# Kernel optimization log

Measured on AMD Instinct MI355X. Metric: run time of the kernel, lower is better.

Reference implementation:

```python
import jax, jax.numpy as jnp
import numpy as np

EPS = 1e-5

def _act_quant(x):
    # per-token int8 absmax quantization with straight-through estimator
    scale = 127.0 / jnp.clip(jnp.max(jnp.abs(x), axis=-1, keepdims=True), EPS, None)
    q = jnp.clip(jnp.round(x * scale), -128.0, 127.0) / scale
    return x + jax.lax.stop_gradient(q - x)

def _weight_quant(w):
    # per-tensor ternary (1.58-bit) quantization with STE
    scale = 1.0 / jnp.clip(jnp.mean(jnp.abs(w)), EPS, None)
    q = jnp.clip(jnp.round(w * scale), -1.0, 1.0) / scale
    return w + jax.lax.stop_gradient(q - w)

def _bitlinear(x, w, b):
    y = jnp.einsum('bsd,od->bso', _act_quant(x), _weight_quant(w))
    return y + b

def setup_inputs() -> dict:
    key = jax.random.key(0)
    k1, k2, k3, k4, k5 = jax.random.split(key, 5)
    B, S, D, F = 8, 4096, 1024, 3072
    return {
        'x': jax.random.normal(k1, (B, S, D), dtype=jnp.float32),
        'up_w': jax.random.normal(k2, (F, D), dtype=jnp.float32) * 0.125,
        'up_b': jax.random.normal(k3, (F,), dtype=jnp.float32) * 0.01,
        'down_w': jax.random.normal(k4, (D, F), dtype=jnp.float32) * 0.125,
        'down_b': jax.random.normal(k5, (D,), dtype=jnp.float32) * 0.01,
    }

def reference(x, up_w, up_b, down_w, down_b):
    hidden = _bitlinear(x, up_w, up_b)          # [B,S,3072]
    hidden = jnp.square(jax.nn.relu(hidden))    # relu(h)^2
    return _bitlinear(hidden, down_w, down_b)   # [B,S,1024]
```

## Files before the change

kernel.cpp:

```cpp
#include <hip/hip_runtime.h>
#include <hip/hip_bf16.h>
#include <stdint.h>

#define EPS 1e-5f

typedef int v4i __attribute__((ext_vector_type(4)));
typedef int v16i __attribute__((ext_vector_type(16)));
typedef const __attribute__((address_space(1))) void g_void;
typedef __attribute__((address_space(3))) void l_void;

__device__ inline float block_max_nw(float v, int nw) {
    __shared__ float s[8];
#pragma unroll
    for (int o = 32; o; o >>= 1) v = fmaxf(v, __shfl_xor(v, o, 64));
    if ((threadIdx.x & 63) == 0) s[threadIdx.x >> 6] = v;
    __syncthreads();
    float m = s[0];
    for (int i = 1; i < nw; ++i) m = fmaxf(m, s[i]);
    return m;
}

__device__ inline float block_sum64x4(float v) {
    __shared__ float s[4];
#pragma unroll
    for (int o = 32; o; o >>= 1) v += __shfl_xor(v, o, 64);
    if ((threadIdx.x & 63) == 0) s[threadIdx.x >> 6] = v;
    __syncthreads();
    return s[0] + s[1] + s[2] + s[3];
}

__global__ __launch_bounds__(256) void abs_sum_part_k(const float4* __restrict__ w,
                                                      int n4, float* __restrict__ part) {
    float s = 0.0f;
    for (int i = blockIdx.x * 256 + threadIdx.x; i < n4; i += 1024 * 256) {
        float4 v = w[i];
        s += fabsf(v.x) + fabsf(v.y) + fabsf(v.z) + fabsf(v.w);
    }
    s = block_sum64x4(s);
    if (threadIdx.x == 0) part[blockIdx.x] = s;
}

__global__ __launch_bounds__(256) void abs_sum_final_k(const float* __restrict__ parts,
                                                       float* __restrict__ sums) {
    const float* p = parts + blockIdx.x * 1024;
    const int t = threadIdx.x;
    float s = p[t] + p[t + 256] + p[t + 512] + p[t + 768];
    s = block_sum64x4(s);
    if (t == 0) sums[blockIdx.x] = s;
}

__global__ __launch_bounds__(256) void wquant_k(const float4* __restrict__ w,
                                                char4* __restrict__ q,
                                                const float* __restrict__ sum) {
    const float mean = fmaxf(sum[0] * (1.0f / 3145728.0f), EPS);
    const float scale = 1.0f / mean;
    const int i = blockIdx.x * 256 + threadIdx.x;
    float4 v = w[i];
    char4 c;
    c.x = (signed char)(int)fmaxf(fminf(rintf(v.x * scale), 1.0f), -1.0f);
    c.y = (signed char)(int)fmaxf(fminf(rintf(v.y * scale), 1.0f), -1.0f);
    c.z = (signed char)(int)fmaxf(fminf(rintf(v.z * scale), 1.0f), -1.0f);
    c.w = (signed char)(int)fmaxf(fminf(rintf(v.w * scale), 1.0f), -1.0f);
    q[i] = c;
}

__global__ __launch_bounds__(256) void aquant_k(const float4* __restrict__ x,
                                                char4* __restrict__ q,
                                                float* __restrict__ deq) {
    const int row = blockIdx.x, t = threadIdx.x;
    const float4 v = x[(size_t)row * 256 + t];
    float m = fmaxf(fmaxf(fabsf(v.x), fabsf(v.y)), fmaxf(fabsf(v.z), fabsf(v.w)));
    m = block_max_nw(m, 4);
    const float mc = fmaxf(m, EPS);
    const float sc = 127.0f / mc;
    char4 c;
    c.x = (signed char)(int)fmaxf(fminf(rintf(v.x * sc), 127.0f), -128.0f);
    c.y = (signed char)(int)fmaxf(fminf(rintf(v.y * sc), 127.0f), -128.0f);
    c.z = (signed char)(int)fmaxf(fminf(rintf(v.z * sc), 127.0f), -128.0f);
    c.w = (signed char)(int)fmaxf(fminf(rintf(v.w * sc), 127.0f), -128.0f);
    q[(size_t)row * 256 + t] = c;
    if (t == 0) deq[row] = mc / 127.0f;
}

__global__ __launch_bounds__(384) void hquant_k(unsigned short* __restrict__ hid,
                                                float* __restrict__ deq) {
    const size_t row = blockIdx.x;
    const int t = threadIdx.x;
    unsigned short* rp = hid + row * 3072;
    const uint4 u = ((const uint4*)rp)[t];
    float v[8];
    {
        uint32_t uu[4] = {u.x, u.y, u.z, u.w};
#pragma unroll
        for (int i = 0; i < 4; ++i) {
            uint32_t lo = uu[i] << 16, hi = uu[i] & 0xFFFF0000u;
            v[2 * i]     = __uint_as_float(lo);
            v[2 * i + 1] = __uint_as_float(hi);
        }
    }
    float m = 0.0f;
#pragma unroll
    for (int i = 0; i < 8; ++i) m = fmaxf(m, fabsf(v[i]));
    m = block_max_nw(m, 6);
    const float mc = fmaxf(m, EPS);
    const float sc = 127.0f / mc;
    uint32_t p0 = 0, p1 = 0;
#pragma unroll
    for (int i = 0; i < 4; ++i) {
        int c = (int)fminf(rintf(v[i] * sc), 127.0f);
        p0 |= (uint32_t)(c & 255) << (8 * i);
    }
#pragma unroll
    for (int i = 0; i < 4; ++i) {
        int c = (int)fminf(rintf(v[4 + i] * sc), 127.0f);
        p1 |= (uint32_t)(c & 255) << (8 * i);
    }
    uint2 pk; pk.x = p0; pk.y = p1;
    ((uint2*)rp)[t] = pk;
    if (t == 0) deq[row] = mc / 127.0f;
}

template <bool RELU2, typename OutT>
__global__ __launch_bounds__(256, 2) void gemm_i8(
    const int8_t* __restrict__ A, int lda,
    const int8_t* __restrict__ B, int ldb,
    OutT* __restrict__ O, int ldo,
    const float* __restrict__ rowDeq,
    const float* __restrict__ sumPtr,
    const float* __restrict__ bias,
    int K, int nTiles) {
    __shared__ __align__(16) char As[128 * 128];
    __shared__ __align__(16) char Bs[256 * 128];
    const int t = threadIdx.x;
    const int lane = t & 63;
    const int w = t >> 6;
    const int xcd = blockIdx.x & 7;
    const int s = blockIdx.x >> 3;
    const int bm = xcd + 8 * (s / nTiles);
    const int bn = s % nTiles;
    const long m0 = (long)bm * 128;
    const long n0 = (long)bn * 256;

    v16i acc[2][4];
#pragma unroll
    for (int i = 0; i < 2; ++i)
#pragma unroll
        for (int j = 0; j < 4; ++j) acc[i][j] = (v16i)(0);

    const int mloc = (w >> 1) * 64;
    const int nloc = (w & 1) * 128;
    const int r32 = lane & 31;
    const int h = lane >> 5;
    const int swz = r32 & 7;
    const int srow = lane >> 3;
    const int scol = ((lane & 7) ^ srow) * 16;

    const int8_t* pa = A + (m0 + w * 8 + srow) * (long)lda + scol;
    const int8_t* pb = B + (n0 + w * 8 + srow) * (long)ldb + scol;

    int cs[4];
#pragma unroll
    for (int ks = 0; ks < 4; ++ks) cs[ks] = ((ks * 2 + h) ^ swz) * 16;

    for (int k0 = 0; k0 < K; k0 += 128) {
#pragma unroll
        for (int r = 0; r < 4; ++r)
            __builtin_amdgcn_global_load_lds((g_void*)(pa + (long)r * 32 * lda + k0),
                                             (l_void*)(As + r * 4096 + w * 1024), 16, 0, 0);
#pragma unroll
        for (int r = 0; r < 8; ++r)
            __builtin_amdgcn_global_load_lds((g_void*)(pb + (long)r * 32 * ldb + k0),
                                             (l_void*)(Bs + r * 4096 + w * 1024), 16, 0, 0);
        __syncthreads();
#pragma unroll
        for (int ks = 0; ks < 4; ++ks) {
            v4i af[2], bf[4];
#pragma unroll
            for (int mt = 0; mt < 2; ++mt)
                af[mt] = *(const v4i*)(As + (mloc + mt * 32 + r32) * 128 + cs[ks]);
#pragma unroll
            for (int nt = 0; nt < 4; ++nt)
                bf[nt] = *(const v4i*)(Bs + (nloc + nt * 32 + r32) * 128 + cs[ks]);
#pragma unroll
            for (int mt = 0; mt < 2; ++mt)
#pragma unroll
                for (int nt = 0; nt < 4; ++nt)
                    acc[mt][nt] = __builtin_amdgcn_mfma_i32_32x32x32_i8(
                        af[mt], bf[nt], acc[mt][nt], 0, 0, 0);
        }
        __syncthreads();
    }

    const float wdeq = fmaxf(sumPtr[0] * (1.0f / 3145728.0f), EPS);
#pragma unroll
    for (int mt = 0; mt < 2; ++mt) {
#pragma unroll
        for (int g = 0; g < 4; ++g) {
#pragma unroll
            for (int rr = 0; rr < 4; ++rr) {
                const long row = m0 + mloc + mt * 32 + g * 8 + h * 4 + rr;
                const float rs = rowDeq[row] * wdeq;
#pragma unroll
                for (int nt = 0; nt < 4; ++nt) {
                    const long col = n0 + nloc + nt * 32 + r32;
                    float val = (float)acc[mt][nt][g * 4 + rr] * rs + bias[col];
                    if (RELU2) {
                        val = fmaxf(val, 0.0f);
                        val = val * val;
                    }
                    O[row * (long)ldo + col] = (OutT)val;
                }
            }
        }
    }
}

extern "C" void kernel_launch(void* const* d_in, const int* in_sizes, int n_in,
                              void* d_out, int out_size, void* d_ws, size_t ws_size,
                              hipStream_t stream) {
    const float* x      = (const float*)d_in[0];
    const float* up_w   = (const float*)d_in[1];
    const float* up_b   = (const float*)d_in[2];
    const float* down_w = (const float*)d_in[3];
    const float* down_b = (const float*)d_in[4];

    char* ws = (char*)d_ws;
    float*  sums   = (float*)ws;
    float*  parts  = (float*)(ws + 256);
    int8_t* qw_dn  = (int8_t*)(ws + 256 + 8192);
    float*  deqh   = (float*)(ws + 256 + 8192 + 3145728);
    __hip_bfloat16* hidden = (__hip_bfloat16*)(ws + 256 + 8192 + 3145728 + 131072);

    int8_t* qx    = (int8_t*)d_out;
    int8_t* qw_up = qx + 33554432;
    float*  deqx  = (float*)(qx + 33554432 + 3145728);

    abs_sum_part_k<<<1024, 256, 0, stream>>>((const float4*)up_w, 786432, parts);
    abs_sum_part_k<<<1024, 256, 0, stream>>>((const float4*)down_w, 786432, parts + 1024);
    abs_sum_final_k<<<2, 256, 0, stream>>>(parts, sums);

    wquant_k<<<3072, 256, 0, stream>>>((const float4*)up_w, (char4*)qw_up, &sums[0]);
    wquant_k<<<3072, 256, 0, stream>>>((const float4*)down_w, (char4*)qw_dn, &sums[1]);
    aquant_k<<<32768, 256, 0, stream>>>((const float4*)x, (char4*)qx, deqx);

    gemm_i8<true, __hip_bfloat16><<<3072, 256, 0, stream>>>(
        qx, 1024, qw_up, 1024, hidden, 3072, deqx, &sums[0], up_b, 1024, 12);
    hquant_k<<<32768, 384, 0, stream>>>((unsigned short*)hidden, deqh);
    gemm_i8<false, float><<<1024, 256, 0, stream>>>(
        (const int8_t*)hidden, 6144, qw_dn, 3072, (float*)d_out, 1024,
        deqh, &sums[1], down_b, 3072, 4);
}
```

Measured before the change: 537.6 us.

## Enlarge int8 GEMM tile to 256x256 with 8 waves and double-buffered LDS prefetch

```diff
diff --git a/kernel.cpp b/kernel.cpp
--- a/kernel.cpp
+++ b/kernel.cpp
@@ -121,7 +121,7 @@
 }
 
 template <bool RELU2, typename OutT>
-__global__ __launch_bounds__(256, 2) void gemm_i8(
+__global__ __launch_bounds__(512, 2) void gemm_i8(
     const int8_t* __restrict__ A, int lda,
     const int8_t* __restrict__ B, int ldb,
     OutT* __restrict__ O, int ldo,
@@ -129,31 +129,33 @@
     const float* __restrict__ sumPtr,
     const float* __restrict__ bias,
     int K, int nTiles) {
-    __shared__ __align__(16) char As[128 * 128];
-    __shared__ __align__(16) char Bs[256 * 128];
+    __shared__ __align__(16) char As[2][32768];
+    __shared__ __align__(16) char Bs[2][32768];
     const int t = threadIdx.x;
     const int lane = t & 63;
     const int w = t >> 6;
+    const int wm = w >> 2;
+    const int wn = w & 3;
     const int xcd = blockIdx.x & 7;
-    const int s = blockIdx.x >> 3;
-    const int bm = xcd + 8 * (s / nTiles);
-    const int bn = s % nTiles;
-    const long m0 = (long)bm * 128;
+    const int sb = blockIdx.x >> 3;
+    const int bm = xcd + 8 * (sb / nTiles);
+    const int bn = sb % nTiles;
+    const long m0 = (long)bm * 256;
     const long n0 = (long)bn * 256;
 
-    v16i acc[2][4];
-#pragma unroll
-    for (int i = 0; i < 2; ++i)
-#pragma unroll
-        for (int j = 0; j < 4; ++j) acc[i][j] = (v16i)(0);
-
-    const int mloc = (w >> 1) * 64;
-    const int nloc = (w & 1) * 128;
+    v16i acc[4][2];
+#pragma unroll
+    for (int i = 0; i < 4; ++i)
+#pragma unroll
+        for (int j = 0; j < 2; ++j) acc[i][j] = (v16i)(0);
+
     const int r32 = lane & 31;
     const int h = lane >> 5;
     const int swz = r32 & 7;
     const int srow = lane >> 3;
     const int scol = ((lane & 7) ^ srow) * 16;
+    const int mloc = wm * 128;
+    const int nloc = wn * 64;
 
     const int8_t* pa = A + (m0 + w * 8 + srow) * (long)lda + scol;
     const int8_t* pb = B + (n0 + w * 8 + srow) * (long)ldb + scol;
@@ -162,38 +164,62 @@
 #pragma unroll
     for (int ks = 0; ks < 4; ++ks) cs[ks] = ((ks * 2 + h) ^ swz) * 16;
 
-    for (int k0 = 0; k0 < K; k0 += 128) {
+    const int NT = K >> 7;
+
+    auto STAGE = [&](int tt, int buf) {
+        const long ko = (long)tt << 7;
 #pragma unroll
         for (int r = 0; r < 4; ++r)
-            __builtin_amdgcn_global_load_lds((g_void*)(pa + (long)r * 32 * lda + k0),
-                                             (l_void*)(As + r * 4096 + w * 1024), 16, 0, 0);
-#pragma unroll
-        for (int r = 0; r < 8; ++r)
-            __builtin_amdgcn_global_load_lds((g_void*)(pb + (long)r * 32 * ldb + k0),
-                                             (l_void*)(Bs + r * 4096 + w * 1024), 16, 0, 0);
-        __syncthreads();
+            __builtin_amdgcn_global_load_lds((g_void*)(pa + (long)(r * 64) * lda + ko),
+                                             (l_void*)(As[buf] + r * 8192 + w * 1024), 16, 0, 0);
+#pragma unroll
+        for (int r = 0; r < 4; ++r)
+            __builtin_amdgcn_global_load_lds((g_void*)(pb + (long)(r * 64) * ldb + ko),
+                                             (l_void*)(Bs[buf] + r * 8192 + w * 1024), 16, 0, 0);
+    };
+
+    STAGE(0, 0);
+    STAGE(1, 1);
+    asm volatile("s_waitcnt vmcnt(8)" ::: "memory");
+    __builtin_amdgcn_s_barrier();
+    asm volatile("" ::: "memory");
+
+    for (int tt = 0; tt < NT; ++tt) {
+        const int cur = tt & 1;
+        v4i af[4][4], bf[2][4];
 #pragma unroll
         for (int ks = 0; ks < 4; ++ks) {
-            v4i af[2], bf[4];
-#pragma unroll
-            for (int mt = 0; mt < 2; ++mt)
-                af[mt] = *(const v4i*)(As + (mloc + mt * 32 + r32) * 128 + cs[ks]);
-#pragma unroll
-            for (int nt = 0; nt < 4; ++nt)
-                bf[nt] = *(const v4i*)(Bs + (nloc + nt * 32 + r32) * 128 + cs[ks]);
-#pragma unroll
-            for (int mt = 0; mt < 2; ++mt)
-#pragma unroll
-                for (int nt = 0; nt < 4; ++nt)
+#pragma unroll
+            for (int mt = 0; mt < 4; ++mt)
+                af[mt][ks] = *(const v4i*)(As[cur] + (mloc + mt * 32 + r32) * 128 + cs[ks]);
+#pragma unroll
+            for (int nt = 0; nt < 2; ++nt)
+                bf[nt][ks] = *(const v4i*)(Bs[cur] + (nloc + nt * 32 + r32) * 128 + cs[ks]);
+        }
+        asm volatile("s_waitcnt lgkmcnt(0)" ::: "memory");
+        __builtin_amdgcn_s_barrier();
+        asm volatile("" ::: "memory");
+        const bool pf = (tt + 2 < NT);
+        if (pf) STAGE(tt + 2, cur);
+        __builtin_amdgcn_s_setprio(1);
+#pragma unroll
+        for (int ks = 0; ks < 4; ++ks)
+#pragma unroll
+            for (int mt = 0; mt < 4; ++mt)
+#pragma unroll
+                for (int nt = 0; nt < 2; ++nt)
                     acc[mt][nt] = __builtin_amdgcn_mfma_i32_32x32x32_i8(
-                        af[mt], bf[nt], acc[mt][nt], 0, 0, 0);
-        }
-        __syncthreads();
+                        af[mt][ks], bf[nt][ks], acc[mt][nt], 0, 0, 0);
+        __builtin_amdgcn_s_setprio(0);
+        if (pf) asm volatile("s_waitcnt vmcnt(8)" ::: "memory");
+        else    asm volatile("s_waitcnt vmcnt(0)" ::: "memory");
+        __builtin_amdgcn_s_barrier();
+        asm volatile("" ::: "memory");
     }
 
     const float wdeq = fmaxf(sumPtr[0] * (1.0f / 3145728.0f), EPS);
 #pragma unroll
-    for (int mt = 0; mt < 2; ++mt) {
+    for (int mt = 0; mt < 4; ++mt) {
 #pragma unroll
         for (int g = 0; g < 4; ++g) {
 #pragma unroll
@@ -201,7 +227,7 @@
                 const long row = m0 + mloc + mt * 32 + g * 8 + h * 4 + rr;
                 const float rs = rowDeq[row] * wdeq;
 #pragma unroll
-                for (int nt = 0; nt < 4; ++nt) {
+                for (int nt = 0; nt < 2; ++nt) {
                     const long col = n0 + nloc + nt * 32 + r32;
                     float val = (float)acc[mt][nt][g * 4 + rr] * rs + bias[col];
                     if (RELU2) {
@@ -243,10 +269,10 @@
     wquant_k<<<3072, 256, 0, stream>>>((const float4*)down_w, (char4*)qw_dn, &sums[1]);
     aquant_k<<<32768, 256, 0, stream>>>((const float4*)x, (char4*)qx, deqx);
 
-    gemm_i8<true, __hip_bfloat16><<<3072, 256, 0, stream>>>(
+    gemm_i8<true, __hip_bfloat16><<<1536, 512, 0, stream>>>(
         qx, 1024, qw_up, 1024, hidden, 3072, deqx, &sums[0], up_b, 1024, 12);
     hquant_k<<<32768, 384, 0, stream>>>((unsigned short*)hidden, deqh);
-    gemm_i8<false, float><<<1024, 256, 0, stream>>>(
+    gemm_i8<false, float><<<512, 512, 0, stream>>>(
         (const int8_t*)hidden, 6144, qw_dn, 3072, (float*)d_out, 1024,
         deqh, &sums[1], down_b, 3072, 4);
 }
```

Result: slower. 582.3 us (+8.3%).

## Triple-buffer int8 GEMM LDS tiles with async prefetch and single barrier per step

Applied to the files above, without the earlier changes.

```diff
diff --git a/kernel.cpp b/kernel.cpp
--- a/kernel.cpp
+++ b/kernel.cpp
@@ -129,15 +129,14 @@
     const float* __restrict__ sumPtr,
     const float* __restrict__ bias,
     int K, int nTiles) {
-    __shared__ __align__(16) char As[128 * 128];
-    __shared__ __align__(16) char Bs[256 * 128];
+    __shared__ __align__(16) char lds[3][24576];
     const int t = threadIdx.x;
     const int lane = t & 63;
     const int w = t >> 6;
     const int xcd = blockIdx.x & 7;
-    const int s = blockIdx.x >> 3;
-    const int bm = xcd + 8 * (s / nTiles);
-    const int bn = s % nTiles;
+    const int sb = blockIdx.x >> 3;
+    const int bm = xcd + 8 * (sb / nTiles);
+    const int bn = sb % nTiles;
     const long m0 = (long)bm * 128;
     const long n0 = (long)bn * 256;
 
@@ -151,44 +150,68 @@
     const int nloc = (w & 1) * 128;
     const int r32 = lane & 31;
     const int h = lane >> 5;
-    const int swz = r32 & 7;
-    const int srow = lane >> 3;
-    const int scol = ((lane & 7) ^ srow) * 16;
-
-    const int8_t* pa = A + (m0 + w * 8 + srow) * (long)lda + scol;
-    const int8_t* pb = B + (n0 + w * 8 + srow) * (long)ldb + scol;
-
-    int cs[4];
-#pragma unroll
-    for (int ks = 0; ks < 4; ++ks) cs[ks] = ((ks * 2 + h) ^ swz) * 16;
-
-    for (int k0 = 0; k0 < K; k0 += 128) {
+
+    const int srow = lane >> 2;
+    const int sc = ((lane & 3) ^ ((lane >> 3) & 3)) * 16;
+    const int8_t* paS = A + (m0 + w * 32 + srow) * (long)lda + sc;
+    const int8_t* pbS = B + (n0 + w * 64 + srow) * (long)ldb + sc;
+
+    int cro[2];
+#pragma unroll
+    for (int ks = 0; ks < 2; ++ks) cro[ks] = ((2 * ks + h) ^ ((r32 >> 1) & 3)) * 16;
+
+    const int NT = K >> 6;
+
+    auto STAGE = [&](int tt) {
+        char* buf = lds[tt % 3];
+        const long ko = (long)tt << 6;
+#pragma unroll
+        for (int r = 0; r < 2; ++r)
+            __builtin_amdgcn_global_load_lds(
+                (g_void*)(paS + (long)(r * 16) * lda + ko),
+                (l_void*)(buf + w * 2048 + r * 1024 + lane * 16), 16, 0, 0);
 #pragma unroll
         for (int r = 0; r < 4; ++r)
-            __builtin_amdgcn_global_load_lds((g_void*)(pa + (long)r * 32 * lda + k0),
-                                             (l_void*)(As + r * 4096 + w * 1024), 16, 0, 0);
-#pragma unroll
-        for (int r = 0; r < 8; ++r)
-            __builtin_amdgcn_global_load_lds((g_void*)(pb + (long)r * 32 * ldb + k0),
-                                             (l_void*)(Bs + r * 4096 + w * 1024), 16, 0, 0);
-        __syncthreads();
-#pragma unroll
-        for (int ks = 0; ks < 4; ++ks) {
+            __builtin_amdgcn_global_load_lds(
+                (g_void*)(pbS + (long)(r * 16) * ldb + ko),
+                (l_void*)(buf + 8192 + w * 4096 + r * 1024 + lane * 16), 16, 0, 0);
+    };
+
+    STAGE(0);
+    STAGE(1);
+    asm volatile("s_waitcnt vmcnt(6)" ::: "memory");
+    __builtin_amdgcn_s_barrier();
+    __builtin_amdgcn_sched_barrier(0);
+
+    for (int tt = 0; tt < NT; ++tt) {
+        const char* buf = lds[tt % 3];
+        const bool pf = (tt + 2 < NT);
+        if (pf) STAGE(tt + 2);
+        __builtin_amdgcn_sched_barrier(0);
+#pragma unroll
+        for (int ks = 0; ks < 2; ++ks) {
             v4i af[2], bf[4];
 #pragma unroll
             for (int mt = 0; mt < 2; ++mt)
-                af[mt] = *(const v4i*)(As + (mloc + mt * 32 + r32) * 128 + cs[ks]);
+                af[mt] = *(const v4i*)(buf + (mloc + mt * 32 + r32) * 64 + cro[ks]);
 #pragma unroll
             for (int nt = 0; nt < 4; ++nt)
-                bf[nt] = *(const v4i*)(Bs + (nloc + nt * 32 + r32) * 128 + cs[ks]);
+                bf[nt] = *(const v4i*)(buf + 8192 + (nloc + nt * 32 + r32) * 64 + cro[ks]);
+            __builtin_amdgcn_s_setprio(1);
 #pragma unroll
             for (int mt = 0; mt < 2; ++mt)
 #pragma unroll
                 for (int nt = 0; nt < 4; ++nt)
                     acc[mt][nt] = __builtin_amdgcn_mfma_i32_32x32x32_i8(
                         af[mt], bf[nt], acc[mt][nt], 0, 0, 0);
-        }
-        __syncthreads();
+            __builtin_amdgcn_s_setprio(0);
+        }
+        if (tt + 1 < NT) {
+            if (pf) asm volatile("s_waitcnt vmcnt(6)" ::: "memory");
+            else    asm volatile("s_waitcnt vmcnt(0)" ::: "memory");
+            __builtin_amdgcn_s_barrier();
+            __builtin_amdgcn_sched_barrier(0);
+        }
     }
 
     const float wdeq = fmaxf(sumPtr[0] * (1.0f / 3145728.0f), EPS);
```

Result: no change. 538.0 us (+0.1%).
